# Kernel tuning notes

Hardware: AMD Instinct MI355X
Metric: run time of the kernel (lower is better)

The kernel has to match this reference:

```python
import jax, jax.numpy as jnp
import numpy as np

EPS = 1e-7  # tf.keras.backend.epsilon()
ROUTING_ITERS = 3


def setup_inputs() -> dict:
    key = jax.random.key(0)
    k1, k2 = jax.random.split(key)
    B, I, Din = 64, 4096, 8
    N, D = 10, 16
    inputs = jax.random.normal(k1, (B, I, Din), dtype=jnp.float32)
    # glorot_uniform-ish init for W [I, N, Din, D]
    limit = (6.0 / (Din + D)) ** 0.5
    W = jax.random.uniform(k2, (I, N, Din, D), dtype=jnp.float32, minval=-limit, maxval=limit)
    return {"inputs": inputs, "W": W}


def _elementwise_squash(s):
    # Original squashes over axis=-2 of [B,1,N,1,D], a size-1 axis ->
    # the reduce_sum is a no-op and squash becomes elementwise.
    sq = s * s
    scale = sq / (1.0 + sq) / jnp.sqrt(sq + EPS)
    return scale * s


def reference(inputs, W):
    # inputs: [B, I, Din], W: [I, N, Din, D]
    # u_hat[b,i,n,d] = sum_p inputs[b,i,p] * W[i,n,p,d]  (the tile+matmul)
    u_hat = jnp.einsum('bip,inpd->bind', inputs, W)  # [B, I, N, D]
    B, I, N, D = u_hat.shape
    b = jnp.zeros((B, I, N, 1), dtype=u_hat.dtype)
    v = None
    for it in range(ROUTING_ITERS):
        c = jax.nn.softmax(b, axis=2)                 # [B, I, N, 1]
        s = jnp.sum(c * u_hat, axis=1)                # [B, N, D]
        v = _elementwise_squash(s)                    # [B, N, D]
        if it < ROUTING_ITERS - 1:
            # agreement: sum over D -> [B, I, N, 1]
            b = b + jnp.sum(u_hat * v[:, None, :, :], axis=-1, keepdims=True)
    # original: squeeze(v[B,1,N,1,D], axis=1) -> [B, N, 1, D]
    return v[:, :, None, :]
```

## Files before the change

kernel.cpp:

```cpp
#include <hip/hip_runtime.h>
#include <math.h>

#define B_ 64
#define I_ 4096
#define P_ 8
#define N_ 10
#define D_ 16
#define ND_ 160
#define BND_ (B_*ND_)
#define EPS_ 1e-7f

#define IPB_ 8
#define NBLK_ (I_ / IPB_)
#define WTILE_ (N_ * P_ * D_)
#define NSTR_ 144
#define ILSTR_ (N_ * NSTR_)
#define XSTR_ 68

#define NGRP_ 16
#define GSZ_  32
#define LINEW_ 16
#define SLOTW_ ((NGRP_ + 1) * LINEW_)
#define NSLOT_ 5

template<int CTRL>
__device__ __forceinline__ float dpp_bcast(float v) {
    int r = __builtin_amdgcn_update_dpp(0, __float_as_int(v), CTRL, 0xF, 0xF, true);
    return __int_as_float(r);
}

__device__ __forceinline__ void agent_store_f2(float* dst, float a, float b) {
    float2 v; v.x = a; v.y = b;
    unsigned long long u; __builtin_memcpy(&u, &v, 8);
    __hip_atomic_store((unsigned long long*)dst, u,
                       __ATOMIC_RELAXED, __HIP_MEMORY_SCOPE_AGENT);
}
__device__ __forceinline__ float2 agent_load_f2(const float* src) {
    unsigned long long u = __hip_atomic_load((unsigned long long*)src,
                       __ATOMIC_RELAXED, __HIP_MEMORY_SCOPE_AGENT);
    float2 v; __builtin_memcpy(&v, &u, 8); return v;
}
__device__ __forceinline__ void agent_store_f(float* dst, float v) {
    __hip_atomic_store(dst, v, __ATOMIC_RELAXED, __HIP_MEMORY_SCOPE_AGENT);
}

__device__ __forceinline__ void gridbar(unsigned* cnt, int slot) {
    __syncthreads();
    if (threadIdx.x == 0) {
        unsigned* base = cnt + slot * SLOTW_;
        const unsigned g = (unsigned)blockIdx.x & (NGRP_ - 1u);
        unsigned* gl = base + g * LINEW_;
        unsigned* rp = base + NGRP_ * LINEW_;
        __builtin_amdgcn_fence(__ATOMIC_RELEASE, "workgroup");
        unsigned gold = __hip_atomic_fetch_add(&gl[0], 1u,
                            __ATOMIC_RELAXED, __HIP_MEMORY_SCOPE_AGENT);
        unsigned epoch = gold / (unsigned)GSZ_;
        if ((gold % (unsigned)GSZ_) == (unsigned)GSZ_ - 1u)
            __hip_atomic_fetch_add(&rp[0], 1u,
                __ATOMIC_RELAXED, __HIP_MEMORY_SCOPE_AGENT);
        long long t0 = (long long)__builtin_amdgcn_s_memrealtime();
        if ((unsigned)blockIdx.x < (unsigned)NGRP_) {
            unsigned rtgt = (epoch + 1u) * (unsigned)NGRP_;
            while (__hip_atomic_load(&rp[0], __ATOMIC_RELAXED,
                                     __HIP_MEMORY_SCOPE_AGENT) < rtgt) {
                __builtin_amdgcn_s_sleep(1);
                if ((long long)__builtin_amdgcn_s_memrealtime() - t0 > 2000000LL)
                    break;
            }
            __hip_atomic_store(&gl[1], epoch + 1u,
                __ATOMIC_RELAXED, __HIP_MEMORY_SCOPE_AGENT);
        } else {
            while (__hip_atomic_load(&gl[1], __ATOMIC_RELAXED,
                                     __HIP_MEMORY_SCOPE_AGENT) < epoch + 1u) {
                __builtin_amdgcn_s_sleep(1);
                if ((long long)__builtin_amdgcn_s_memrealtime() - t0 > 2000000LL)
                    break;
            }
        }
        __builtin_amdgcn_fence(__ATOMIC_ACQUIRE, "workgroup");
    }
    __syncthreads();
}

__global__ __launch_bounds__(256, 2)
void digitcaps_fused(const float* __restrict__ x, const float* __restrict__ W,
                     float* __restrict__ part, float* __restrict__ Vc,
                     float* __restrict__ out, unsigned* __restrict__ cnt)
{
    __shared__ float wsh[IPB_ * ILSTR_];
    __shared__ float xsh[B_ * XSTR_];
    __shared__ float4 rsm4[48][5];
    const int t = threadIdx.x;
    const int lane = t & 63;
    const int ds  = lane & 7;
    const int np  = (lane >> 3) & 1;
    const int bl2 = lane >> 4;
    const int wv  = t >> 6;
    const int bb  = wv * 16 + bl2 * 4;
    const int i0  = blockIdx.x * IPB_;

    {
        const float4* __restrict__ Wg = (const float4*)(W + (size_t)i0 * WTILE_);
        float4* __restrict__ Ws = (float4*)wsh;
#pragma unroll
        for (int c0 = 0; c0 < (IPB_ * WTILE_) / (4 * 256); ++c0) {
            int c  = c0 * 256 + t;
            int il = c / 320;
            int r  = c - il * 320;
            int n  = r >> 5;
            int s  = r & 31;
            Ws[il * 360 + n * 36 + s] = Wg[c];
        }
    }
    {
        const int xb = t >> 2;
        const int xc = t & 3;
        const float4* __restrict__ xg = (const float4*)(x + ((size_t)xb * I_ + i0) * P_);
        float4* __restrict__ xd = (float4*)(xsh + xb * XSTR_);
#pragma unroll
        for (int q = 0; q < 4; ++q)
            xd[xc * 4 + q] = xg[xc * 4 + q];
    }
    __syncthreads();

    float vprev = 0.f;

    for (int it = 0; it < 3; ++it) {
        const bool uni = (it == 0);

        float vc[4][5][2];
        if (!uni) {
#pragma unroll
            for (int j = 0; j < 4; ++j)
#pragma unroll
                for (int k = 0; k < 5; ++k) {
                    float2 v = agent_load_f2(Vc + (size_t)(bb + j) * ND_
                                             + (np + 2 * k) * D_ + 2 * ds);
                    vc[j][k][0] = v.x; vc[j][k][1] = v.y;
                }
        }

        float acc[4][5][2];
#pragma unroll
        for (int j = 0; j < 4; ++j)
#pragma unroll
            for (int k = 0; k < 5; ++k) { acc[j][k][0] = 0.f; acc[j][k][1] = 0.f; }

#pragma unroll 1
        for (int il = 0; il < IPB_; ++il) {
            const float* __restrict__ Wb = wsh + il * ILSTR_ + np * NSTR_ + 2 * ds;

            float xr[4][P_];
#pragma unroll
            for (int j = 0; j < 4; ++j) {
                const float4* xp = (const float4*)(xsh + (bb + j) * XSTR_ + il * P_);
                float4 a0 = xp[0], a1 = xp[1];
                xr[j][0]=a0.x; xr[j][1]=a0.y; xr[j][2]=a0.z; xr[j][3]=a0.w;
                xr[j][4]=a1.x; xr[j][5]=a1.y; xr[j][6]=a1.z; xr[j][7]=a1.w;
            }

            float tv[4][5][2];
#pragma unroll
            for (int k = 0; k < 5; ++k) {
#pragma unroll
                for (int j = 0; j < 4; ++j) { tv[j][k][0] = 0.f; tv[j][k][1] = 0.f; }
#pragma unroll
                for (int p = 0; p < P_; ++p) {
                    float2 w = *(const float2*)(Wb + k * 2 * NSTR_ + p * D_);
#pragma unroll
                    for (int j = 0; j < 4; ++j) {
                        tv[j][k][0] = fmaf(w.x, xr[j][p], tv[j][k][0]);
                        tv[j][k][1] = fmaf(w.y, xr[j][p], tv[j][k][1]);
                    }
                }
            }

            if (uni) {
#pragma unroll
                for (int j = 0; j < 4; ++j)
#pragma unroll
                    for (int k = 0; k < 5; ++k) {
                        acc[j][k][0] += tv[j][k][0];
                        acc[j][k][1] += tv[j][k][1];
                    }
            } else {
#pragma unroll
                for (int j = 0; j < 4; ++j) {
                    float e[5];
                    float m = -1e30f;
#pragma unroll
                    for (int k = 0; k < 5; ++k) {
                        float l = fmaf(tv[j][k][1], vc[j][k][1],
                                       tv[j][k][0] * vc[j][k][0]);
                        l += dpp_bcast<0xB1>(l);
                        l += dpp_bcast<0x4E>(l);
                        l += dpp_bcast<0x141>(l);
                        e[k] = l;
                        m = fmaxf(m, l);
                    }
                    m = fmaxf(m, dpp_bcast<0x140>(m));
                    float se = 0.f;
#pragma unroll
                    for (int k = 0; k < 5; ++k) { e[k] = __expf(e[k] - m); se += e[k]; }
                    se += dpp_bcast<0x140>(se);
                    float inv = 1.f / se;
#pragma unroll
                    for (int k = 0; k < 5; ++k) {
                        float cn = e[k] * inv;
                        acc[j][k][0] = fmaf(cn, tv[j][k][0], acc[j][k][0]);
                        acc[j][k][1] = fmaf(cn, tv[j][k][1], acc[j][k][1]);
                    }
                }
            }
        }

#pragma unroll
        for (int j = 0; j < 4; ++j) {
            float* __restrict__ dst = part + (size_t)blockIdx.x * BND_
                                      + (size_t)(bb + j) * ND_ + np * D_ + 2 * ds;
#pragma unroll
            for (int k = 0; k < 5; ++k)
                agent_store_f2(dst + k * 2 * D_, acc[j][k][0], acc[j][k][1]);
        }

        gridbar(cnt, it * 2);

        const int o0 = blockIdx.x * 20;
        if (t < 240) {
            const int fg = t % 5;
            const int tp = t / 5;
            const int r0 = (tp < 32) ? tp * 11 : 352 + (tp - 32) * 10;
            const int rc = (tp < 32) ? 11 : 10;
            float4 s4 = {0.f, 0.f, 0.f, 0.f};
            const float* __restrict__ p0 = part + (size_t)r0 * BND_ + o0 + fg * 4;
            for (int r = 0; r < rc; ++r) {
                float2 a = agent_load_f2(p0 + (size_t)r * BND_);
                float2 b = agent_load_f2(p0 + (size_t)r * BND_ + 2);
                s4.x += a.x; s4.y += a.y; s4.z += b.x; s4.w += b.y;
            }
            rsm4[tp][fg] = s4;
        }
        __syncthreads();
        if (t < 20) {
            const int fg = t >> 2, c = t & 3;
            float tot = 0.f;
#pragma unroll
            for (int tp = 0; tp < 48; ++tp)
                tot += ((const float*)&rsm4[tp][fg])[c];
            tot *= uni ? 0.1f : 1.0f;
            float sq = tot * tot;
            float v = tot * (sq / ((1.f + sq) * sqrtf(sq + EPS_)));
            const int o2 = o0 + t;
            if (it == 0)      { vprev = v;   agent_store_f(Vc + o2, vprev); }
            else if (it == 1) { vprev += v;  agent_store_f(Vc + o2, vprev); }
            else              out[o2] = v;
        }

        if (it < 2) gridbar(cnt, it * 2 + 1);
    }
}

extern "C" void kernel_launch(void* const* d_in, const int* in_sizes, int n_in,
                              void* d_out, int out_size, void* d_ws, size_t ws_size,
                              hipStream_t stream)
{
    const float* x = (const float*)d_in[0];
    const float* W = (const float*)d_in[1];
    float* out = (float*)d_out;

    float* part = (float*)d_ws;
    float* Vc   = part + (size_t)NBLK_ * BND_;
    unsigned* cnt = (unsigned*)(Vc + BND_);

    hipMemsetAsync(cnt, 0, NSLOT_ * SLOTW_ * sizeof(unsigned), stream);

    digitcaps_fused<<<dim3(NBLK_), dim3(256), 0, stream>>>(x, W, part, Vc, out, cnt);
}
```

Measured before the change: 169.9 us.

## Split grid barrier into arrive/wait, overlap first tile compute, pad partial stride

Splits the second grid barrier of each routing iteration into arrive and wait halves, so each block computes the first input capsule's u_hat before waiting for the updated V. It also pads the per-block partial buffer stride (10240 to 10304 floats) to avoid channel/bank aliasing. The cross-block reduction now uses 160 threads, each issuing 16 batched loads before summing, instead of 240 threads with serial loops. This hides some barrier latency and increases memory-level parallelism, at the cost of more registers and fewer reducing threads.

```diff
diff --git a/kernel.cpp b/kernel.cpp
--- a/kernel.cpp
+++ b/kernel.cpp
@@ -8,6 +8,7 @@
 #define D_ 16
 #define ND_ 160
 #define BND_ (B_*ND_)
+#define PSTR_ 10304
 #define EPS_ 1e-7f
 
 #define IPB_ 8
@@ -44,8 +45,9 @@
     __hip_atomic_store(dst, v, __ATOMIC_RELAXED, __HIP_MEMORY_SCOPE_AGENT);
 }
 
-__device__ __forceinline__ void gridbar(unsigned* cnt, int slot) {
+__device__ __forceinline__ unsigned gridbar_arrive(unsigned* cnt, int slot) {
     __syncthreads();
+    unsigned epoch = 0;
     if (threadIdx.x == 0) {
         unsigned* base = cnt + slot * SLOTW_;
         const unsigned g = (unsigned)blockIdx.x & (NGRP_ - 1u);
@@ -54,10 +56,20 @@
         __builtin_amdgcn_fence(__ATOMIC_RELEASE, "workgroup");
         unsigned gold = __hip_atomic_fetch_add(&gl[0], 1u,
                             __ATOMIC_RELAXED, __HIP_MEMORY_SCOPE_AGENT);
-        unsigned epoch = gold / (unsigned)GSZ_;
+        epoch = gold / (unsigned)GSZ_;
         if ((gold % (unsigned)GSZ_) == (unsigned)GSZ_ - 1u)
             __hip_atomic_fetch_add(&rp[0], 1u,
                 __ATOMIC_RELAXED, __HIP_MEMORY_SCOPE_AGENT);
+    }
+    return epoch;
+}
+
+__device__ __forceinline__ void gridbar_wait(unsigned* cnt, int slot, unsigned epoch) {
+    if (threadIdx.x == 0) {
+        unsigned* base = cnt + slot * SLOTW_;
+        const unsigned g = (unsigned)blockIdx.x & (NGRP_ - 1u);
+        unsigned* gl = base + g * LINEW_;
+        unsigned* rp = base + NGRP_ * LINEW_;
         long long t0 = (long long)__builtin_amdgcn_s_memrealtime();
         if ((unsigned)blockIdx.x < (unsigned)NGRP_) {
             unsigned rtgt = (epoch + 1u) * (unsigned)NGRP_;
@@ -89,7 +101,7 @@
 {
     __shared__ float wsh[IPB_ * ILSTR_];
     __shared__ float xsh[B_ * XSTR_];
-    __shared__ float4 rsm4[48][5];
+    __shared__ float4 rsm4[32][5];
     const int t = threadIdx.x;
     const int lane = t & 63;
     const int ds  = lane & 7;
@@ -123,13 +135,50 @@
     }
     __syncthreads();
 
+    auto compute_tv = [&](int il, float (&tv)[4][5][2]) {
+        const float* __restrict__ Wb = wsh + il * ILSTR_ + np * NSTR_ + 2 * ds;
+        float xr[4][P_];
+#pragma unroll
+        for (int j = 0; j < 4; ++j) {
+            const float4* xp = (const float4*)(xsh + (bb + j) * XSTR_ + il * P_);
+            float4 a0 = xp[0], a1 = xp[1];
+            xr[j][0]=a0.x; xr[j][1]=a0.y; xr[j][2]=a0.z; xr[j][3]=a0.w;
+            xr[j][4]=a1.x; xr[j][5]=a1.y; xr[j][6]=a1.z; xr[j][7]=a1.w;
+        }
+#pragma unroll
+        for (int k = 0; k < 5; ++k) {
+#pragma unroll
+            for (int j = 0; j < 4; ++j) { tv[j][k][0] = 0.f; tv[j][k][1] = 0.f; }
+#pragma unroll
+            for (int p = 0; p < P_; ++p) {
+                float2 w = *(const float2*)(Wb + k * 2 * NSTR_ + p * D_);
+#pragma unroll
+                for (int j = 0; j < 4; ++j) {
+                    tv[j][k][0] = fmaf(w.x, xr[j][p], tv[j][k][0]);
+                    tv[j][k][1] = fmaf(w.y, xr[j][p], tv[j][k][1]);
+                }
+            }
+        }
+    };
+
     float vprev = 0.f;
+    unsigned epO = 0;
 
     for (int it = 0; it < 3; ++it) {
         const bool uni = (it == 0);
 
+        float acc[4][5][2];
+#pragma unroll
+        for (int j = 0; j < 4; ++j)
+#pragma unroll
+            for (int k = 0; k < 5; ++k) { acc[j][k][0] = 0.f; acc[j][k][1] = 0.f; }
+
         float vc[4][5][2];
+        float tv[4][5][2];
+
+        compute_tv(0, tv);
         if (!uni) {
+            gridbar_wait(cnt, (it - 1) * 2 + 1, epO);
 #pragma unroll
             for (int j = 0; j < 4; ++j)
 #pragma unroll
@@ -140,40 +189,9 @@
                 }
         }
 
-        float acc[4][5][2];
-#pragma unroll
-        for (int j = 0; j < 4; ++j)
-#pragma unroll
-            for (int k = 0; k < 5; ++k) { acc[j][k][0] = 0.f; acc[j][k][1] = 0.f; }
-
 #pragma unroll 1
         for (int il = 0; il < IPB_; ++il) {
-            const float* __restrict__ Wb = wsh + il * ILSTR_ + np * NSTR_ + 2 * ds;
-
-            float xr[4][P_];
-#pragma unroll
-            for (int j = 0; j < 4; ++j) {
-                const float4* xp = (const float4*)(xsh + (bb + j) * XSTR_ + il * P_);
-                float4 a0 = xp[0], a1 = xp[1];
-                xr[j][0]=a0.x; xr[j][1]=a0.y; xr[j][2]=a0.z; xr[j][3]=a0.w;
-                xr[j][4]=a1.x; xr[j][5]=a1.y; xr[j][6]=a1.z; xr[j][7]=a1.w;
-            }
-
-            float tv[4][5][2];
-#pragma unroll
-            for (int k = 0; k < 5; ++k) {
-#pragma unroll
-                for (int j = 0; j < 4; ++j) { tv[j][k][0] = 0.f; tv[j][k][1] = 0.f; }
-#pragma unroll
-                for (int p = 0; p < P_; ++p) {
-                    float2 w = *(const float2*)(Wb + k * 2 * NSTR_ + p * D_);
-#pragma unroll
-                    for (int j = 0; j < 4; ++j) {
-                        tv[j][k][0] = fmaf(w.x, xr[j][p], tv[j][k][0]);
-                        tv[j][k][1] = fmaf(w.y, xr[j][p], tv[j][k][1]);
-                    }
-                }
-            }
+            if (il > 0) compute_tv(il, tv);
 
             if (uni) {
 #pragma unroll
@@ -216,27 +234,35 @@
 
 #pragma unroll
         for (int j = 0; j < 4; ++j) {
-            float* __restrict__ dst = part + (size_t)blockIdx.x * BND_
+            float* __restrict__ dst = part + (size_t)blockIdx.x * PSTR_
                                       + (size_t)(bb + j) * ND_ + np * D_ + 2 * ds;
 #pragma unroll
             for (int k = 0; k < 5; ++k)
                 agent_store_f2(dst + k * 2 * D_, acc[j][k][0], acc[j][k][1]);
         }
 
-        gridbar(cnt, it * 2);
+        {
+            unsigned epE = gridbar_arrive(cnt, it * 2);
+            gridbar_wait(cnt, it * 2, epE);
+        }
 
         const int o0 = blockIdx.x * 20;
-        if (t < 240) {
+        if (t < 160) {
             const int fg = t % 5;
             const int tp = t / 5;
-            const int r0 = (tp < 32) ? tp * 11 : 352 + (tp - 32) * 10;
-            const int rc = (tp < 32) ? 11 : 10;
+            const float* __restrict__ p0 = part + (size_t)(tp * 16) * PSTR_
+                                           + o0 + fg * 4;
+            float2 va[32];
+#pragma unroll
+            for (int r = 0; r < 16; ++r) {
+                va[2*r]   = agent_load_f2(p0 + (size_t)r * PSTR_);
+                va[2*r+1] = agent_load_f2(p0 + (size_t)r * PSTR_ + 2);
+            }
             float4 s4 = {0.f, 0.f, 0.f, 0.f};
-            const float* __restrict__ p0 = part + (size_t)r0 * BND_ + o0 + fg * 4;
-            for (int r = 0; r < rc; ++r) {
-                float2 a = agent_load_f2(p0 + (size_t)r * BND_);
-                float2 b = agent_load_f2(p0 + (size_t)r * BND_ + 2);
-                s4.x += a.x; s4.y += a.y; s4.z += b.x; s4.w += b.y;
+#pragma unroll
+            for (int r = 0; r < 16; ++r) {
+                s4.x += va[2*r].x;   s4.y += va[2*r].y;
+                s4.z += va[2*r+1].x; s4.w += va[2*r+1].y;
             }
             rsm4[tp][fg] = s4;
         }
@@ -245,7 +271,7 @@
             const int fg = t >> 2, c = t & 3;
             float tot = 0.f;
 #pragma unroll
-            for (int tp = 0; tp < 48; ++tp)
+            for (int tp = 0; tp < 32; ++tp)
                 tot += ((const float*)&rsm4[tp][fg])[c];
             tot *= uni ? 0.1f : 1.0f;
             float sq = tot * tot;
@@ -256,7 +282,7 @@
             else              out[o2] = v;
         }
 
-        if (it < 2) gridbar(cnt, it * 2 + 1);
+        if (it < 2) epO = gridbar_arrive(cnt, it * 2 + 1);
     }
 }
 
@@ -269,7 +295,7 @@
     float* out = (float*)d_out;
 
     float* part = (float*)d_ws;
-    float* Vc   = part + (size_t)NBLK_ * BND_;
+    float* Vc   = part + (size_t)NBLK_ * PSTR_;
     unsigned* cnt = (unsigned*)(Vc + BND_);
 
     hipMemsetAsync(cnt, 0, NSLOT_ * SLOTW_ * sizeof(unsigned), stream);
```

Result: no change. 171.9 us (+1.2%).
